# Kernel optimization log

Hardware: AMD Instinct MI355X
Metric: run time of the kernel (lower is better)

Reference implementation:

```python
import jax, jax.numpy as jnp
import numpy as np

P, C, D = 65536, 64, 256

def setup_inputs() -> dict:
    key = jax.random.key(0)
    k1, k2, k3, k4 = jax.random.split(key, 4)
    return {
        "protos1": jax.random.normal(k1, (P, D), dtype=jnp.float32),
        "protos2": jax.random.normal(k2, (P, D), dtype=jnp.float32),
        "W": jax.random.normal(k3, (D, D), dtype=jnp.float32) / np.float32(np.sqrt(D)),
        "b": jax.random.normal(k4, (D,), dtype=jnp.float32),
        "num_classes": C,
    }

def _pairwise_dist(x, y):
    # x: (C, n, D), y: (C, m, D) -> squared-euclidean-style dists (C, n, m)
    xs = jnp.sum(x * x, axis=-1)[:, :, None]
    ys = jnp.sum(y * y, axis=-1)[:, None, :]
    return xs + ys - 2.0 * jnp.einsum('cid,cjd->cij', x, y)

def reference(protos1, protos2, W, b, num_classes):
    nc = int(num_classes)
    d = protos1.shape[-1]
    # prototypes[c::num_classes] for all c at once: (P,D) -> (P//C, C, D) -> (C, P//C, D)
    p1 = protos1.reshape(-1, nc, d).transpose(1, 0, 2)
    p2 = protos2.reshape(-1, nc, d).transpose(1, 0, 2)
    # transition: nn.Linear -> x @ W.T + b ; inverse: (x - b) @ inv(W.T)
    p2_inv = (p2 - b) @ jnp.linalg.inv(W.T)
    p1_fwd = p1 @ W.T + b
    a = _pairwise_dist(p1, p2_inv)          # (C, n, n)
    bb = _pairwise_dist(p2, p1_fwd)         # (C, n, n)
    proto_losses_source = jnp.mean(jnp.min(a, axis=2), axis=1)   # (C,)
    proto_losses_target = jnp.mean(jnp.min(bb, axis=2), axis=1)  # (C,)
    return jnp.stack([proto_losses_source, proto_losses_target])  # (2, C)
```

## Files before the change

kernel.cpp:

```cpp
#include <hip/hip_runtime.h>

#define D 256
#define NC 64

using u16 = unsigned short;
using u32 = unsigned int;

typedef __attribute__((ext_vector_type(8))) short bfv8;
typedef __attribute__((ext_vector_type(4))) float f32x4;
typedef __attribute__((ext_vector_type(2))) int v2i;

__device__ __forceinline__ float bf2f(u32 u) {
  union { u32 i; float f; } v; v.i = u << 16; return v.f;
}
__device__ __forceinline__ u16 f2bf(float f) {
  union { float f; u32 i; } v; v.f = f;
  u32 x = v.i;
  return (u16)((x + 0x7FFFu + ((x >> 16) & 1u)) >> 16);
}
__device__ __forceinline__ u32 pk2(float a, float b) {
  return (u32)f2bf(a) | ((u32)f2bf(b) << 16);
}
__device__ __forceinline__ size_t cmrow(int g) {
  return (size_t)(((g & 63) << 10) | (g >> 6));
}

__device__ __forceinline__ void gload_lds16(const void* src, void* dst) {
  __builtin_amdgcn_global_load_lds(
      (const __attribute__((address_space(1))) void*)src,
      (__attribute__((address_space(3))) void*)dst, 16, 0, 0);
}

#define K1_LDS 71168
#define DISTP_LDS 70144

__device__ void gj_body(const float* __restrict__ W, float* __restrict__ IW,
                        char* smem) {
  float (*Ml)[20]    = (float(*)[20])smem;
  float (*Arow)[256] = (float(*)[256])(smem + 20480);
  float (*G)[256]    = (float(*)[256])(smem + 36864);
  u16*  Gfrag        = (u16*)(smem + 53248);
  float (*Pinv)[20]  = (float(*)[20])(smem + 69888);
  const int t = threadIdx.x, w = t >> 6, l = t & 63;
  const int lj = l & 15, lh = l >> 4;
  const int r0 = 16 * w;
  const bool lo32 = (l < 32);

  f32x4 x[16];
#pragma unroll
  for (int ct = 0; ct < 16; ++ct)
#pragma unroll
    for (int reg = 0; reg < 4; ++reg)
      x[ct][reg] = W[(size_t)(r0 + 4 * lh + reg) * D + 16 * ct + lj];

  for (int s = 0; s < 16; ++s) {
#pragma unroll
    for (int ct = 0; ct < 16; ++ct)
      if (ct == s)
#pragma unroll
        for (int reg = 0; reg < 4; ++reg)
          Ml[r0 + 4 * lh + reg][lj] = x[ct][reg];
    if (w == s) {
#pragma unroll
      for (int ct = 0; ct < 16; ++ct)
#pragma unroll
        for (int reg = 0; reg < 4; ++reg)
          Arow[4 * lh + reg][16 * ct + lj] = x[ct][reg];
    }
    bfv8 afr;
    {
      const int row = r0 + lj;
      float4 f0 = *(const float4*)&Ml[row][8 * (lh & 1)];
      float4 f1 = *(const float4*)&Ml[row][8 * (lh & 1) + 4];
      const float fv[8] = {f0.x, f0.y, f0.z, f0.w, f1.x, f1.y, f1.z, f1.w};
      union { bfv8 v; u16 e[8]; } A;
      if (lh < 2) {
#pragma unroll
        for (int e = 0; e < 8; ++e) A.e[e] = f2bf(-fv[e]);
      } else {
#pragma unroll
        for (int e = 0; e < 8; ++e) {
          const float hi = bf2f(f2bf(fv[e]));
          A.e[e] = f2bf(-(fv[e] - hi));
        }
      }
      afr = A.v;
    }
    __syncthreads();
    if (t < 16) {
      float p[16];
      {
        float4 rr0 = *(const float4*)&Ml[16 * s + t][0];
        float4 rr1 = *(const float4*)&Ml[16 * s + t][4];
        float4 rr2 = *(const float4*)&Ml[16 * s + t][8];
        float4 rr3 = *(const float4*)&Ml[16 * s + t][12];
        p[0] = rr0.x; p[1] = rr0.y; p[2] = rr0.z; p[3] = rr0.w;
        p[4] = rr1.x; p[5] = rr1.y; p[6] = rr1.z; p[7] = rr1.w;
        p[8] = rr2.x; p[9] = rr2.y; p[10] = rr2.z; p[11] = rr2.w;
        p[12] = rr3.x; p[13] = rr3.y; p[14] = rr3.z; p[15] = rr3.w;
      }
#pragma unroll
      for (int pp = 0; pp < 16; ++pp) {
        float u[16];
#pragma unroll
        for (int j = 0; j < 16; ++j)
          u[j] = __int_as_float(__builtin_amdgcn_readlane(__float_as_int(p[j]), pp));
        const float pv = u[pp];
        const float d = 1.0f / pv;
        if (t == pp) {
#pragma unroll
          for (int j = 0; j < 16; ++j) p[j] = u[j] * d;
          p[pp] = d;
        } else {
          const float md = p[pp] * d;
          u[pp] = pv + 1.0f;
#pragma unroll
          for (int j = 0; j < 16; ++j) p[j] = fmaf(-md, u[j], p[j]);
        }
      }
#pragma unroll
      for (int j = 0; j < 16; ++j) Pinv[t][j] = p[j];
    }
    __syncthreads();
    {
      const bool inC = ((l >> 2) == s);
      const int co = (l & 3) << 2;
      const int gct = l >> 2;
      const int kk = w;
      float4 g = make_float4(0.f, 0.f, 0.f, 0.f);
#pragma unroll
      for (int q = 0; q < 16; ++q) {
        const float pv = Pinv[kk][q];
        const float4 av = *(const float4*)&Arow[q][4 * l];
        g.x = fmaf(pv, av.x, g.x); g.y = fmaf(pv, av.y, g.y);
        g.z = fmaf(pv, av.z, g.z); g.w = fmaf(pv, av.w, g.w);
      }
      if (inC) {
        g.x = Pinv[kk][co + 0] + (kk == co + 0 ? 1.f : 0.f);
        g.y = Pinv[kk][co + 1] + (kk == co + 1 ? 1.f : 0.f);
        g.z = Pinv[kk][co + 2] + (kk == co + 2 ? 1.f : 0.f);
        g.w = Pinv[kk][co + 3] + (kk == co + 3 ? 1.f : 0.f);
      }
      *(float4*)&G[kk][4 * l] = g;
      const int e0 = kk & 7;
      const int lbase = 16 * (kk >> 3);
      const float gv[4] = {g.x, g.y, g.z, g.w};
#pragma unroll
      for (int cc = 0; cc < 4; ++cc) {
        const int cl = 4 * (l & 3) + cc;
        const u16 hi = f2bf(gv[cc]);
        const u16 lo = f2bf(gv[cc] - bf2f(hi));
        Gfrag[gct * 520 + (lbase + cl) * 8 + e0] = hi;
        Gfrag[gct * 520 + (32 + lbase + cl) * 8 + e0] = lo;
      }
    }
    __syncthreads();
    if (w != s) {
#pragma unroll
      for (int ct = 0; ct < 16; ++ct) {
        union { bfv8 v; uint4 u; } B1, B2;
        B1.v = *(const bfv8*)&Gfrag[ct * 520 + l * 8];
#if __has_builtin(__builtin_amdgcn_permlane32_swap)
        {
          v2i r;
          r = __builtin_amdgcn_permlane32_swap((int)B1.u.x, (int)B1.u.x, false, false);
          B2.u.x = lo32 ? (u32)r.y : (u32)r.x;
          r = __builtin_amdgcn_permlane32_swap((int)B1.u.y, (int)B1.u.y, false, false);
          B2.u.y = lo32 ? (u32)r.y : (u32)r.x;
          r = __builtin_amdgcn_permlane32_swap((int)B1.u.z, (int)B1.u.z, false, false);
          B2.u.z = lo32 ? (u32)r.y : (u32)r.x;
          r = __builtin_amdgcn_permlane32_swap((int)B1.u.w, (int)B1.u.w, false, false);
          B2.u.w = lo32 ? (u32)r.y : (u32)r.x;
        }
#else
        B2.v = *(const bfv8*)&Gfrag[ct * 520 + (l ^ 32) * 8];
#endif
        x[ct] = __builtin_amdgcn_mfma_f32_16x16x32_bf16(afr, B1.v, x[ct], 0, 0, 0);
        x[ct] = __builtin_amdgcn_mfma_f32_16x16x32_bf16(afr, B2.v, x[ct], 0, 0, 0);
      }
    } else {
#pragma unroll
      for (int ct = 0; ct < 16; ++ct) {
        if (ct == s) {
#pragma unroll
          for (int reg = 0; reg < 4; ++reg)
            x[ct][reg] = Pinv[4 * lh + reg][lj];
        } else {
#pragma unroll
          for (int reg = 0; reg < 4; ++reg)
            x[ct][reg] = G[4 * lh + reg][16 * ct + lj];
        }
      }
    }
    __syncthreads();
  }
#pragma unroll
  for (int ct = 0; ct < 16; ++ct)
#pragma unroll
    for (int reg = 0; reg < 4; ++reg)
      IW[(size_t)(r0 + 4 * lh + reg) * D + 16 * ct + lj] = x[ct][reg];
}

__device__ void convnorm_role(const float* __restrict__ P, u16* __restrict__ Pb,
                              float* __restrict__ nrm, int blk) {
  const int tx = threadIdx.x;
  const int r = tx >> 2, q = tx & 3;
  const int g = blk * 256 + r;
  const float* src = P + (size_t)g * D + q * 64;
  u16* dst = Pb + cmrow(g) * D + q * 64;
  float ss = 0.f;
#pragma unroll
  for (int g4 = 0; g4 < 8; ++g4) {
    float4 v0 = *(const float4*)(src + g4 * 8);
    float4 v1 = *(const float4*)(src + g4 * 8 + 4);
    ss = fmaf(v0.x, v0.x, fmaf(v0.y, v0.y, fmaf(v0.z, v0.z, fmaf(v0.w, v0.w, ss))));
    ss = fmaf(v1.x, v1.x, fmaf(v1.y, v1.y, fmaf(v1.z, v1.z, fmaf(v1.w, v1.w, ss))));
    uint4 w4;
    w4.x = pk2(v0.x, v0.y); w4.y = pk2(v0.z, v0.w);
    w4.z = pk2(v1.x, v1.y); w4.w = pk2(v1.z, v1.w);
    *(uint4*)(dst + g4 * 8) = w4;
  }
  ss += __shfl_xor(ss, 1, 64);
  ss += __shfl_xor(ss, 2, 64);
  if (q == 0) nrm[cmrow(g)] = ss;
}

template <int MODE>
__device__ void distp_body(const float* __restrict__ Pj,
                           const u16* __restrict__ Brows,
                           const float* __restrict__ biasv,
                           const u16* __restrict__ Pib,
                           const float* __restrict__ nB,
                           float* __restrict__ pmind, int bid, char* smem) {
  const int lb = (bid & 7) * 64 + (bid >> 3);
  const int c = lb >> 3, jt = lb & 7;
  const int tx = threadIdx.x, ww = tx >> 6, l = tx & 63;
  const int mw = ww >> 3, nw = ww & 7, l4 = l >> 4, lm = l & 15;
  char* Ab = smem;
  float* nfpart = (float*)(smem + 65536);
  float* minbuf = (float*)(smem + 65536);
  float* nAb = (float*)(smem + 69632);

  auto issue_chunk = [&](int buf, int ch) {
#pragma unroll
    for (int u = 0; u < 2; ++u) {
      const int chunk = ww * 2 + u, ks = chunk >> 2, n = chunk & 3;
      const u16* src = Pib + ((size_t)(c << 10) + ch * 64 + n * 16 + lm) * D
                       + ks * 32 + l4 * 8;
      gload_lds16(src, Ab + buf * 32768 + chunk * 1024);
    }
  };

  bfv8 bfr[2][8];
#pragma unroll
  for (int nf2 = 0; nf2 < 2; ++nf2)
#pragma unroll
    for (int ks = 0; ks < 8; ++ks)
      bfr[nf2][ks] = *(const bfv8*)(Brows +
          (size_t)(nw * 32 + nf2 * 16 + lm) * D + ks * 32 + l4 * 8);
  {
    const int r = tx >> 3, sg = tx & 7;
    const float* arow = Pj + ((size_t)(jt * 128 + r) * NC + c) * D + sg * 32;
#pragma unroll
    for (int g2 = 0; g2 < 4; ++g2) {
      float4 v0 = *(const float4*)(arow + g2 * 8);
      float4 v1 = *(const float4*)(arow + g2 * 8 + 4);
      uint4 w4;
      w4.x = pk2(v0.x, v0.y); w4.y = pk2(v0.z, v0.w);
      w4.z = pk2(v1.x, v1.y); w4.w = pk2(v1.z, v1.w);
      *(uint4*)(Ab + (sg * 8 + (r >> 4)) * 1024 + ((r & 15) + g2 * 16) * 16) = w4;
    }
  }
  __syncthreads();
  const bfv8* A8 = (const bfv8*)Ab;
  f32x4 acc[4][2];
#pragma unroll
  for (int mf = 0; mf < 4; ++mf) {
    acc[mf][0] = f32x4{0.f, 0.f, 0.f, 0.f};
    acc[mf][1] = f32x4{0.f, 0.f, 0.f, 0.f};
  }
#pragma unroll
  for (int ks = 0; ks < 8; ++ks)
#pragma unroll
    for (int mf = 0; mf < 4; ++mf) {
      bfv8 a = A8[(ks * 8 + mw * 4 + mf) * 64 + l];
      acc[mf][0] = __builtin_amdgcn_mfma_f32_16x16x32_bf16(a, bfr[0][ks], acc[mf][0], 0, 0, 0);
      acc[mf][1] = __builtin_amdgcn_mfma_f32_16x16x32_bf16(a, bfr[1][ks], acc[mf][1], 0, 0, 0);
    }
  float bias[2];
  if (MODE == 0) {
#pragma unroll
    for (int nf2 = 0; nf2 < 2; ++nf2)
      bias[nf2] = biasv[nw * 32 + nf2 * 16 + lm];
  } else {
#pragma unroll
    for (int nf2 = 0; nf2 < 2; ++nf2) {
      float pd = 0.f;
#pragma unroll
      for (int ks = 0; ks < 8; ++ks) {
        float4 b0 = *(const float4*)(biasv + ks * 32 + l4 * 8);
        float4 b1 = *(const float4*)(biasv + ks * 32 + l4 * 8 + 4);
        pd = fmaf(b0.x, bf2f((u16)bfr[nf2][ks][0]), pd);
        pd = fmaf(b0.y, bf2f((u16)bfr[nf2][ks][1]), pd);
        pd = fmaf(b0.z, bf2f((u16)bfr[nf2][ks][2]), pd);
        pd = fmaf(b0.w, bf2f((u16)bfr[nf2][ks][3]), pd);
        pd = fmaf(b1.x, bf2f((u16)bfr[nf2][ks][4]), pd);
        pd = fmaf(b1.y, bf2f((u16)bfr[nf2][ks][5]), pd);
        pd = fmaf(b1.z, bf2f((u16)bfr[nf2][ks][6]), pd);
        pd = fmaf(b1.w, bf2f((u16)bfr[nf2][ks][7]), pd);
      }
      pd += __shfl_xor(pd, 16, 64);
      pd += __shfl_xor(pd, 32, 64);
      bias[nf2] = -pd;
    }
  }
  __syncthreads();
  u16* tile = (u16*)Ab;
#pragma unroll
  for (int mf = 0; mf < 4; ++mf)
#pragma unroll
    for (int rr = 0; rr < 4; ++rr) {
      const int j = mw * 64 + mf * 16 + l4 * 4 + rr;
      float v2 = 0.f;
#pragma unroll
      for (int nf2 = 0; nf2 < 2; ++nf2) {
        const float v = acc[mf][nf2][rr] + bias[nf2];
        const u16 hv = f2bf(v);
        tile[(((nw * 8 + mw * 4 + mf) << 6) + ((nf2 * 2 + (lm >> 3)) << 4)
              + l4 * 4 + rr) * 8 + (lm & 7)] = hv;
        const float vr = bf2f(hv);
        v2 = fmaf(vr, vr, v2);
      }
      v2 += __shfl_xor(v2, 1, 64);
      v2 += __shfl_xor(v2, 2, 64);
      v2 += __shfl_xor(v2, 4, 64);
      v2 += __shfl_xor(v2, 8, 64);
      if (lm == 0) nfpart[nw * 128 + j] = v2;
    }
  __syncthreads();
  const int jw = ww >> 2, iw = ww & 3;
  bfv8 afr[2][8];
#pragma unroll
  for (int jj = 0; jj < 2; ++jj)
#pragma unroll
    for (int ks = 0; ks < 8; ++ks)
      afr[jj][ks] = A8[(ks * 8 + jw * 2 + jj) * 64 + l];
  __syncthreads();
  issue_chunk(0, 0);
  if (tx < 128) {
    float s = 0.f;
#pragma unroll
    for (int q = 0; q < 8; ++q) s += nfpart[q * 128 + tx];
    nAb[tx] = s;
  }
  __syncthreads();
  float naj[2][4];
#pragma unroll
  for (int jj = 0; jj < 2; ++jj)
#pragma unroll
    for (int rr = 0; rr < 4; ++rr)
      naj[jj][rr] = nAb[jw * 32 + jj * 16 + l4 * 4 + rr];
  const float* nBc = nB + (c << 10);
  const size_t obase = (size_t)(c * 8 + jt) * 1024;
  for (int ch = 0; ch < 16; ++ch) {
    if (ch < 15) issue_chunk((ch + 1) & 1, ch + 1);
    const bfv8* B8 = (const bfv8*)(Ab + (ch & 1) * 32768);
    f32x4 a2[2];
    a2[0] = f32x4{0.f, 0.f, 0.f, 0.f};
    a2[1] = f32x4{0.f, 0.f, 0.f, 0.f};
#pragma unroll
    for (int ks = 0; ks < 8; ++ks) {
      bfv8 b = B8[(ks * 4 + iw) * 64 + l];
      a2[0] = __builtin_amdgcn_mfma_f32_16x16x32_bf16(afr[0][ks], b, a2[0], 0, 0, 0);
      a2[1] = __builtin_amdgcn_mfma_f32_16x16x32_bf16(afr[1][ks], b, a2[1], 0, 0, 0);
    }
    const float nb = nBc[ch * 64 + iw * 16 + lm];
    float mm = 3.0e38f;
#pragma unroll
    for (int jj = 0; jj < 2; ++jj)
#pragma unroll
      for (int rr = 0; rr < 4; ++rr) {
        const float dd = nb + naj[jj][rr] - 2.0f * a2[jj][rr];
        mm = fminf(mm, dd);
      }
    mm = fminf(mm, __shfl_xor(mm, 16, 64));
    mm = fminf(mm, __shfl_xor(mm, 32, 64));
    if (l4 == 0) minbuf[jw * 64 + iw * 16 + lm] = mm;
    __syncthreads();
    if (tx < 64) {
      float m = minbuf[tx];
#pragma unroll
      for (int q = 1; q < 4; ++q) m = fminf(m, minbuf[q * 64 + tx]);
      pmind[obase + ch * 64 + tx] = m;
    }
    __syncthreads();
  }
}

__global__ __launch_bounds__(1024, 1) void k0_kernel(
    const float* __restrict__ p2, u16* __restrict__ p2b,
    float* __restrict__ n2, const float* __restrict__ W,
    u16* __restrict__ Wb) {
  if (blockIdx.x < 256) {
    convnorm_role(p2, p2b, n2, blockIdx.x);
  } else {
    const int t = threadIdx.x;
#pragma unroll
    for (int k = 0; k < 64; ++k) Wb[k * 1024 + t] = f2bf(W[k * 1024 + t]);
  }
}

__global__ __launch_bounds__(1024, 1) void k1_kernel(
    const float* __restrict__ p1, const float* __restrict__ W,
    const u16* __restrict__ Wb, const float* __restrict__ bv,
    const u16* __restrict__ p2b, const float* __restrict__ n2,
    float* __restrict__ pmin1, float* __restrict__ IWa,
    u16* __restrict__ p1b, float* __restrict__ n1) {
  extern __shared__ char smem[];
  const int b = blockIdx.x;
  if (b == 0) {
    gj_body(W, IWa, smem);
  } else if (b <= 512) {
    distp_body<0>(p1, Wb, bv, p2b, n2, pmin1, b - 1, smem);
  } else {
    convnorm_role(p1, p1b, n1, b - 513);
  }
}

__global__ __launch_bounds__(256) void nr_residual(const float* __restrict__ W,
                                                   const float* __restrict__ X,
                                                   float* __restrict__ R) {
  __shared__ float wrow[D];
  const int i = blockIdx.x, j = threadIdx.x;
  wrow[j] = W[i * D + j];
  __syncthreads();
  float acc = 0.f;
#pragma unroll 8
  for (int k = 0; k < D; ++k) acc = fmaf(wrow[k], X[k * D + j], acc);
  R[i * D + j] = (i == j ? 2.0f : 0.0f) - acc;
}

__global__ __launch_bounds__(256) void nr_mult_bf16(const float* __restrict__ X,
                                                    const float* __restrict__ R,
                                                    u16* __restrict__ Yb) {
  __shared__ float xrow[D];
  const int i = blockIdx.x, j = threadIdx.x;
  xrow[j] = X[i * D + j];
  __syncthreads();
  float acc = 0.f;
#pragma unroll 8
  for (int k = 0; k < D; ++k) acc = fmaf(xrow[k], R[k * D + j], acc);
  Yb[i * D + j] = f2bf(acc);
}

__global__ __launch_bounds__(1024, 1) void k3_kernel(
    const float* __restrict__ p2, const u16* __restrict__ IWb,
    const float* __restrict__ bv, const u16* __restrict__ p1b,
    const float* __restrict__ n1, float* __restrict__ pmin0) {
  extern __shared__ char smem[];
  distp_body<1>(p2, IWb, bv, p1b, n1, pmin0, blockIdx.x, smem);
}

__global__ __launch_bounds__(256) void final_kernel(const float* __restrict__ pmin,
                                                    float* __restrict__ out) {
  __shared__ float ws4[4];
  const int dc = blockIdx.x, tx = threadIdx.x;
  const float* base = pmin + (size_t)dc * 8192;
  float s = 0.f;
#pragma unroll
  for (int t = 0; t < 4; ++t) {
    const int i = t * 256 + tx;
    float m = base[i];
#pragma unroll
    for (int j = 1; j < 8; ++j) m = fminf(m, base[j * 1024 + i]);
    s += m;
  }
#pragma unroll
  for (int off = 32; off; off >>= 1) s += __shfl_xor(s, off, 64);
  if ((tx & 63) == 0) ws4[tx >> 6] = s;
  __syncthreads();
  if (tx == 0)
    out[dc] = (ws4[0] + ws4[1] + ws4[2] + ws4[3]) * (1.0f / 1024.0f);
}

extern "C" void kernel_launch(void* const* d_in, const int* in_sizes, int n_in,
                              void* d_out, int out_size, void* d_ws, size_t ws_size,
                              hipStream_t stream) {
  const float* p1 = (const float*)d_in[0];
  const float* p2 = (const float*)d_in[1];
  const float* W  = (const float*)d_in[2];
  const float* bv = (const float*)d_in[3];
  float* out = (float*)d_out;
  char* ws = (char*)d_ws;
  float* n1  = (float*)(ws);
  float* n2  = (float*)(ws + (256 << 10));
  u16* Wb    = (u16*)(ws + (512 << 10));
  u16* IWb   = (u16*)(ws + (640 << 10));
  float* IWa = (float*)(ws + (768 << 10));
  float* Rt  = (float*)(ws + (1024 << 10));
  float* pmin = (float*)(ws + (1280 << 10));
  u16* p1b   = (u16*)(ws + (6u << 20));
  u16* p2b   = (u16*)(ws + (38u << 20));
  float* pmin0 = pmin;
  float* pmin1 = pmin + 524288;

  hipFuncSetAttribute((const void*)k1_kernel,
                      hipFuncAttributeMaxDynamicSharedMemorySize, K1_LDS);
  hipFuncSetAttribute((const void*)k3_kernel,
                      hipFuncAttributeMaxDynamicSharedMemorySize, DISTP_LDS);

  k0_kernel<<<257, 1024, 0, stream>>>(p2, p2b, n2, W, Wb);
  k1_kernel<<<769, 1024, K1_LDS, stream>>>(p1, W, Wb, bv, p2b, n2,
                                           pmin1, IWa, p1b, n1);
  nr_residual<<<256, 256, 0, stream>>>(W, IWa, Rt);
  nr_mult_bf16<<<256, 256, 0, stream>>>(IWa, Rt, IWb);
  k3_kernel<<<512, 1024, DISTP_LDS, stream>>>(p2, IWb, bv, p1b, n1, pmin0);
  final_kernel<<<128, 256, 0, stream>>>(pmin, out);
}
```

Baseline: 279.0 us.

## Drop p2 preconversion kernel and fuse Newton-Schulz refinement kernels

```diff
diff --git a/kernel.cpp b/kernel.cpp
--- a/kernel.cpp
+++ b/kernel.cpp
@@ -31,7 +31,7 @@
       (__attribute__((address_space(3))) void*)dst, 16, 0, 0);
 }
 
-#define K1_LDS 71168
+#define K1_LDS 74240
 #define DISTP_LDS 70144
 
 __device__ void gj_body(const float* __restrict__ W, float* __restrict__ IW,
@@ -227,9 +227,11 @@
 
 template <int MODE>
 __device__ void distp_body(const float* __restrict__ Pj,
-                           const u16* __restrict__ Brows,
+                           const float* __restrict__ Wf,
+                           const u16* __restrict__ BrowsBF,
                            const float* __restrict__ biasv,
-                           const u16* __restrict__ Pib,
+                           const float* __restrict__ PanF,
+                           const u16* __restrict__ PanBF,
                            const float* __restrict__ nB,
                            float* __restrict__ pmind, int bid, char* smem) {
   const int lb = (bid & 7) * 64 + (bid >> 3);
@@ -240,24 +242,59 @@
   float* nfpart = (float*)(smem + 65536);
   float* minbuf = (float*)(smem + 65536);
   float* nAb = (float*)(smem + 69632);
+  float* nbpart = (float*)(smem + 70144);
 
   auto issue_chunk = [&](int buf, int ch) {
 #pragma unroll
     for (int u = 0; u < 2; ++u) {
       const int chunk = ww * 2 + u, ks = chunk >> 2, n = chunk & 3;
-      const u16* src = Pib + ((size_t)(c << 10) + ch * 64 + n * 16 + lm) * D
+      const u16* src = PanBF + ((size_t)(c << 10) + ch * 64 + n * 16 + lm) * D
                        + ks * 32 + l4 * 8;
       gload_lds16(src, Ab + buf * 32768 + chunk * 1024);
     }
   };
+  auto stage_f32 = [&](int buf, int ch) {
+#pragma unroll
+    for (int u = 0; u < 2; ++u) {
+      const int chunk = ww * 2 + u, ks = chunk >> 2, n = chunk & 3;
+      const int m = ch * 64 + n * 16 + lm;
+      const float* src = PanF + ((size_t)m * 64 + c) * D + ks * 32 + l4 * 8;
+      float4 v0 = *(const float4*)src;
+      float4 v1 = *(const float4*)(src + 4);
+      uint4 w4;
+      w4.x = pk2(v0.x, v0.y); w4.y = pk2(v0.z, v0.w);
+      w4.z = pk2(v1.x, v1.y); w4.w = pk2(v1.z, v1.w);
+      *(uint4*)(Ab + buf * 32768 + chunk * 1024 + l * 16) = w4;
+      float ss = fmaf(v0.x, v0.x, fmaf(v0.y, v0.y, fmaf(v0.z, v0.z, v0.w * v0.w)));
+      ss = fmaf(v1.x, v1.x, fmaf(v1.y, v1.y, fmaf(v1.z, v1.z, fmaf(v1.w, v1.w, ss))));
+      ss += __shfl_xor(ss, 16, 64);
+      ss += __shfl_xor(ss, 32, 64);
+      if (l4 == 0) nbpart[buf * 512 + ks * 64 + n * 16 + lm] = ss;
+    }
+  };
 
   bfv8 bfr[2][8];
-#pragma unroll
-  for (int nf2 = 0; nf2 < 2; ++nf2)
-#pragma unroll
-    for (int ks = 0; ks < 8; ++ks)
-      bfr[nf2][ks] = *(const bfv8*)(Brows +
-          (size_t)(nw * 32 + nf2 * 16 + lm) * D + ks * 32 + l4 * 8);
+  if (MODE == 0) {
+#pragma unroll
+    for (int nf2 = 0; nf2 < 2; ++nf2)
+#pragma unroll
+      for (int ks = 0; ks < 8; ++ks) {
+        const float* wsrc = Wf + (size_t)(nw * 32 + nf2 * 16 + lm) * D + ks * 32 + l4 * 8;
+        float4 b0 = *(const float4*)wsrc;
+        float4 b1 = *(const float4*)(wsrc + 4);
+        union { bfv8 v; uint4 u; } cv;
+        cv.u.x = pk2(b0.x, b0.y); cv.u.y = pk2(b0.z, b0.w);
+        cv.u.z = pk2(b1.x, b1.y); cv.u.w = pk2(b1.z, b1.w);
+        bfr[nf2][ks] = cv.v;
+      }
+  } else {
+#pragma unroll
+    for (int nf2 = 0; nf2 < 2; ++nf2)
+#pragma unroll
+      for (int ks = 0; ks < 8; ++ks)
+        bfr[nf2][ks] = *(const bfv8*)(BrowsBF +
+            (size_t)(nw * 32 + nf2 * 16 + lm) * D + ks * 32 + l4 * 8);
+  }
   {
     const int r = tx >> 3, sg = tx & 7;
     const float* arow = Pj + ((size_t)(jt * 128 + r) * NC + c) * D + sg * 32;
@@ -346,7 +383,7 @@
     for (int ks = 0; ks < 8; ++ks)
       afr[jj][ks] = A8[(ks * 8 + jw * 2 + jj) * 64 + l];
   __syncthreads();
-  issue_chunk(0, 0);
+  if (MODE == 0) stage_f32(0, 0); else issue_chunk(0, 0);
   if (tx < 128) {
     float s = 0.f;
 #pragma unroll
@@ -360,10 +397,13 @@
 #pragma unroll
     for (int rr = 0; rr < 4; ++rr)
       naj[jj][rr] = nAb[jw * 32 + jj * 16 + l4 * 4 + rr];
-  const float* nBc = nB + (c << 10);
+  const float* nBc = (MODE == 1) ? nB + (c << 10) : nullptr;
   const size_t obase = (size_t)(c * 8 + jt) * 1024;
   for (int ch = 0; ch < 16; ++ch) {
-    if (ch < 15) issue_chunk((ch + 1) & 1, ch + 1);
+    if (ch < 15) {
+      if (MODE == 0) stage_f32((ch + 1) & 1, ch + 1);
+      else issue_chunk((ch + 1) & 1, ch + 1);
+    }
     const bfv8* B8 = (const bfv8*)(Ab + (ch & 1) * 32768);
     f32x4 a2[2];
     a2[0] = f32x4{0.f, 0.f, 0.f, 0.f};
@@ -374,7 +414,15 @@
       a2[0] = __builtin_amdgcn_mfma_f32_16x16x32_bf16(afr[0][ks], b, a2[0], 0, 0, 0);
       a2[1] = __builtin_amdgcn_mfma_f32_16x16x32_bf16(afr[1][ks], b, a2[1], 0, 0, 0);
     }
-    const float nb = nBc[ch * 64 + iw * 16 + lm];
+    float nb;
+    if (MODE == 0) {
+      const float* nbp = nbpart + (ch & 1) * 512;
+      nb = nbp[iw * 16 + lm];
+#pragma unroll
+      for (int ks = 1; ks < 8; ++ks) nb += nbp[ks * 64 + iw * 16 + lm];
+    } else {
+      nb = nBc[ch * 64 + iw * 16 + lm];
+    }
     float mm = 3.0e38f;
 #pragma unroll
     for (int jj = 0; jj < 2; ++jj)
@@ -397,23 +445,9 @@
   }
 }
 
-__global__ __launch_bounds__(1024, 1) void k0_kernel(
-    const float* __restrict__ p2, u16* __restrict__ p2b,
-    float* __restrict__ n2, const float* __restrict__ W,
-    u16* __restrict__ Wb) {
-  if (blockIdx.x < 256) {
-    convnorm_role(p2, p2b, n2, blockIdx.x);
-  } else {
-    const int t = threadIdx.x;
-#pragma unroll
-    for (int k = 0; k < 64; ++k) Wb[k * 1024 + t] = f2bf(W[k * 1024 + t]);
-  }
-}
-
 __global__ __launch_bounds__(1024, 1) void k1_kernel(
-    const float* __restrict__ p1, const float* __restrict__ W,
-    const u16* __restrict__ Wb, const float* __restrict__ bv,
-    const u16* __restrict__ p2b, const float* __restrict__ n2,
+    const float* __restrict__ p1, const float* __restrict__ p2,
+    const float* __restrict__ W, const float* __restrict__ bv,
     float* __restrict__ pmin1, float* __restrict__ IWa,
     u16* __restrict__ p1b, float* __restrict__ n1) {
   extern __shared__ char smem[];
@@ -421,36 +455,46 @@
   if (b == 0) {
     gj_body(W, IWa, smem);
   } else if (b <= 512) {
-    distp_body<0>(p1, Wb, bv, p2b, n2, pmin1, b - 1, smem);
+    distp_body<0>(p1, W, nullptr, bv, p2, nullptr, nullptr, pmin1, b - 1, smem);
   } else {
     convnorm_role(p1, p1b, n1, b - 513);
   }
 }
 
-__global__ __launch_bounds__(256) void nr_residual(const float* __restrict__ W,
-                                                   const float* __restrict__ X,
-                                                   float* __restrict__ R) {
-  __shared__ float wrow[D];
-  const int i = blockIdx.x, j = threadIdx.x;
-  wrow[j] = W[i * D + j];
-  __syncthreads();
-  float acc = 0.f;
-#pragma unroll 8
-  for (int k = 0; k < D; ++k) acc = fmaf(wrow[k], X[k * D + j], acc);
-  R[i * D + j] = (i == j ? 2.0f : 0.0f) - acc;
-}
-
-__global__ __launch_bounds__(256) void nr_mult_bf16(const float* __restrict__ X,
-                                                    const float* __restrict__ R,
-                                                    u16* __restrict__ Yb) {
-  __shared__ float xrow[D];
-  const int i = blockIdx.x, j = threadIdx.x;
-  xrow[j] = X[i * D + j];
-  __syncthreads();
-  float acc = 0.f;
-#pragma unroll 8
-  for (int k = 0; k < D; ++k) acc = fmaf(xrow[k], R[k * D + j], acc);
-  Yb[i * D + j] = f2bf(acc);
+__global__ __launch_bounds__(256) void ns_fused(const float* __restrict__ W,
+                                                const float* __restrict__ X,
+                                                u16* __restrict__ Yb) {
+  __shared__ float Xc[256][8];
+  __shared__ float Rc[256][8];
+  const int jc = blockIdx.x * 8, t = threadIdx.x;
+  {
+    float4 xa = *(const float4*)&X[(size_t)t * D + jc];
+    float4 xb = *(const float4*)&X[(size_t)t * D + jc + 4];
+    Xc[t][0] = xa.x; Xc[t][1] = xa.y; Xc[t][2] = xa.z; Xc[t][3] = xa.w;
+    Xc[t][4] = xb.x; Xc[t][5] = xb.y; Xc[t][6] = xb.z; Xc[t][7] = xb.w;
+  }
+  __syncthreads();
+  float r[8] = {0.f, 0.f, 0.f, 0.f, 0.f, 0.f, 0.f, 0.f};
+#pragma unroll 4
+  for (int k = 0; k < D; ++k) {
+    const float wv = W[(size_t)t * D + k];
+#pragma unroll
+    for (int q = 0; q < 8; ++q) r[q] = fmaf(wv, Xc[k][q], r[q]);
+  }
+#pragma unroll
+  for (int q = 0; q < 8; ++q)
+    Rc[t][q] = ((t - jc) == q ? 2.0f : 0.0f) - r[q];
+  __syncthreads();
+  float y[8] = {0.f, 0.f, 0.f, 0.f, 0.f, 0.f, 0.f, 0.f};
+#pragma unroll 4
+  for (int k = 0; k < D; ++k) {
+    const float xv = X[(size_t)t * D + k];
+#pragma unroll
+    for (int q = 0; q < 8; ++q) y[q] = fmaf(xv, Rc[k][q], y[q]);
+  }
+#pragma unroll
+  for (int q = 0; q < 8; ++q)
+    Yb[(size_t)t * D + jc + q] = f2bf(y[q]);
 }
 
 __global__ __launch_bounds__(1024, 1) void k3_kernel(
@@ -458,7 +502,7 @@
     const float* __restrict__ bv, const u16* __restrict__ p1b,
     const float* __restrict__ n1, float* __restrict__ pmin0) {
   extern __shared__ char smem[];
-  distp_body<1>(p2, IWb, bv, p1b, n1, pmin0, blockIdx.x, smem);
+  distp_body<1>(p2, nullptr, IWb, bv, nullptr, p1b, n1, pmin0, blockIdx.x, smem);
 }
 
 __global__ __launch_bounds__(256) void final_kernel(const float* __restrict__ pmin,
@@ -493,14 +537,10 @@
   float* out = (float*)d_out;
   char* ws = (char*)d_ws;
   float* n1  = (float*)(ws);
-  float* n2  = (float*)(ws + (256 << 10));
-  u16* Wb    = (u16*)(ws + (512 << 10));
-  u16* IWb   = (u16*)(ws + (640 << 10));
-  float* IWa = (float*)(ws + (768 << 10));
-  float* Rt  = (float*)(ws + (1024 << 10));
-  float* pmin = (float*)(ws + (1280 << 10));
+  float* IWa = (float*)(ws + (256 << 10));
+  u16* IWb   = (u16*)(ws + (512 << 10));
+  float* pmin = (float*)(ws + (1 << 20));
   u16* p1b   = (u16*)(ws + (6u << 20));
-  u16* p2b   = (u16*)(ws + (38u << 20));
   float* pmin0 = pmin;
   float* pmin1 = pmin + 524288;
 
@@ -509,11 +549,8 @@
   hipFuncSetAttribute((const void*)k3_kernel,
                       hipFuncAttributeMaxDynamicSharedMemorySize, DISTP_LDS);
 
-  k0_kernel<<<257, 1024, 0, stream>>>(p2, p2b, n2, W, Wb);
-  k1_kernel<<<769, 1024, K1_LDS, stream>>>(p1, W, Wb, bv, p2b, n2,
-                                           pmin1, IWa, p1b, n1);
-  nr_residual<<<256, 256, 0, stream>>>(W, IWa, Rt);
-  nr_mult_bf16<<<256, 256, 0, stream>>>(IWa, Rt, IWb);
+  k1_kernel<<<769, 1024, K1_LDS, stream>>>(p1, p2, W, bv, pmin1, IWa, p1b, n1);
+  ns_fused<<<32, 256, 0, stream>>>(W, IWa, IWb);
   k3_kernel<<<512, 1024, DISTP_LDS, stream>>>(p2, IWb, bv, p1b, n1, pmin0);
   final_kernel<<<128, 256, 0, stream>>>(pmin, out);
 }
```

Result: slower. 328.8 us (+17.8%).
